# Kernel tuning notes

Hardware: AMD Instinct MI355X
Metric: run time of the kernel (lower is better)

The kernel has to match this reference:

```python
import jax, jax.numpy as jnp
import numpy as np

B, S, D = 8, 160, 256


def setup_inputs() -> dict:
    key = jax.random.key(0)
    kx, kw, kb = jax.random.split(key, 3)
    x = jax.random.normal(kx, (B, S, D), dtype=jnp.float32)
    # torch nn.Linear(2D, D): weight [D, 2D], bias [D]; store transposed W [2D, D]
    lim = 1.0 / np.sqrt(2 * D)
    W = jax.random.uniform(kw, (2 * D, D), minval=-lim, maxval=lim, dtype=jnp.float32)
    b = jax.random.uniform(kb, (D,), minval=-lim, maxval=lim, dtype=jnp.float32)
    return {"x": x, "W": W, "b": b}


def reference(x, W, b):
    Bsz, Ssz, Dsz = x.shape
    # all i<j pairs in the same order as the nested python loop (i outer, j inner)
    idx_i, idx_j = jnp.triu_indices(Ssz, k=1)  # each [P], P = S(S-1)/2
    # fc_rel(cat(x_i, x_j)) = x_i @ W[:D] + x_j @ W[D:] + b
    Wi, Wj = W[:Dsz], W[Dsz:]
    xa = jnp.einsum('bsd,de->bse', x, Wi)  # [B,S,D]
    xb = jnp.einsum('bsd,de->bse', x, Wj)  # [B,S,D]
    return xa[:, idx_i, :] + xb[:, idx_j, :] + b  # [B,P,D]
```

## Files before the change

### kernel.cpp

```cpp
#include <hip/hip_runtime.h>

#define SS 160
#define DD 256
#define BB 8
#define NPAIR 12720
#define M_TOT (BB * SS)
#define TOTROWS (BB * NPAIR)
#define NWAVES 8192

typedef float vfloat4 __attribute__((ext_vector_type(4)));

__global__ __launch_bounds__(512) void gemm_kernel(const float* __restrict__ x,
                                                   const float* __restrict__ W,
                                                   const float* __restrict__ bias,
                                                   float* __restrict__ y) {
    const int BM = 32, BN = 64, BK = 64;
    __shared__ float As[BK][BM + 1];
    __shared__ float Bs[BK][BN];

    const int n0 = blockIdx.x * BN;
    const int m0 = blockIdx.y * BM;
    const int half = (n0 >= DD) ? 1 : 0;
    const float* Wbase = W + (half ? DD * DD : 0);
    const int ncol0 = n0 - (half ? DD : 0);

    const int tid = threadIdx.x;
    const int tx = tid & 15;
    const int ty = tid >> 4;

    const int ar = tid >> 4;
    const int ac = (tid & 15) << 2;
    const int bkr = tid >> 4;
    const int bnc = (tid & 15) << 2;

    float acc[4] = {0.f, 0.f, 0.f, 0.f};

    for (int k0 = 0; k0 < DD; k0 += BK) {
        float4 av = *(const float4*)(x + (m0 + ar) * DD + k0 + ac);
        float4 b0 = *(const float4*)(Wbase + (k0 + bkr) * DD + ncol0 + bnc);
        float4 b1 = *(const float4*)(Wbase + (k0 + bkr + 32) * DD + ncol0 + bnc);
        __syncthreads();
        As[ac + 0][ar] = av.x;
        As[ac + 1][ar] = av.y;
        As[ac + 2][ar] = av.z;
        As[ac + 3][ar] = av.w;
        *(float4*)(&Bs[bkr][bnc])      = b0;
        *(float4*)(&Bs[bkr + 32][bnc]) = b1;
        __syncthreads();
#pragma unroll
        for (int kk = 0; kk < BK; ++kk) {
            float a = As[kk][ty];
            float4 bv = *(const float4*)(&Bs[kk][tx << 2]);
            acc[0] += a * bv.x; acc[1] += a * bv.y;
            acc[2] += a * bv.z; acc[3] += a * bv.w;
        }
    }

    float4 bias4 = make_float4(0.f, 0.f, 0.f, 0.f);
    if (!half) bias4 = *(const float4*)(bias + ncol0 + (tx << 2));

    float* yout = y + (half ? M_TOT * DD : 0);
    float4 r;
    r.x = acc[0] + bias4.x; r.y = acc[1] + bias4.y;
    r.z = acc[2] + bias4.z; r.w = acc[3] + bias4.w;
    *(float4*)(yout + (m0 + ty) * DD + ncol0 + (tx << 2)) = r;
}

__global__ __launch_bounds__(256) void expand_kernel(const float* __restrict__ y,
                                                     float* __restrict__ out) {
    const int gw   = (blockIdx.x << 2) + (threadIdx.x >> 6);
    const int lane = threadIdx.x & 63;

    int r0 = (int)(((long long)gw * TOTROWS) / NWAVES);
    int r1 = (int)(((long long)(gw + 1) * TOTROWS) / NWAVES);

    int b = (unsigned)r0 / NPAIR;
    int p = r0 - b * NPAIR;

    float disc = sqrtf((float)(101761 - 8 * p));
    int i = (int)((319.0f - disc) * 0.5f);
    if (i < 0) i = 0;
    if (i > SS - 2) i = SS - 2;
    while (i > 0 && (i * (2 * SS - 1 - i)) / 2 > p) --i;
    while (((i + 1) * (2 * SS - 2 - i)) / 2 <= p) ++i;
    int j = i + 1 + p - (i * (2 * SS - 1 - i)) / 2;

    const vfloat4* __restrict__ ya4 = (const vfloat4*)y;
    const vfloat4* __restrict__ yb4 = (const vfloat4*)(y + M_TOT * DD);
    vfloat4* po = (vfloat4*)out + ((long long)r0 << 6) + lane;

    int r = r0;
    while (r < r1) {
        vfloat4 va = ya4[((b * SS + i) << 6) + lane];
        const vfloat4* pb = yb4 + ((b * SS + j) << 6) + lane;
        int run = SS - j;
        if (run > r1 - r) run = r1 - r;
#pragma unroll 2
        for (int t = 0; t < run; ++t) {
            vfloat4 vb = pb[t * 64];
            vfloat4 o = va + vb;
            __builtin_nontemporal_store(o, po);
            po += 64;
        }
        r += run;
        ++i;
        if (i == SS - 1) { ++b; i = 0; }
        j = i + 1;
    }
}

extern "C" void kernel_launch(void* const* d_in, const int* in_sizes, int n_in,
                              void* d_out, int out_size, void* d_ws, size_t ws_size,
                              hipStream_t stream) {
    const float* x    = (const float*)d_in[0];
    const float* W    = (const float*)d_in[1];
    const float* bias = (const float*)d_in[2];
    float* y   = (float*)d_ws;
    float* out = (float*)d_out;

    dim3 gemm_grid(512 / 64, 1280 / 32);
    gemm_kernel<<<gemm_grid, 512, 0, stream>>>(x, W, bias, y);

    expand_kernel<<<NWAVES / 4, 256, 0, stream>>>(y, out);
}
```

Baseline: 133.9 us.

## Use 4x4 register tiling and double-buffered shared memory in projection GEMM

```diff
diff --git a/kernel.cpp b/kernel.cpp
--- a/kernel.cpp
+++ b/kernel.cpp
@@ -10,60 +10,99 @@
 
 typedef float vfloat4 __attribute__((ext_vector_type(4)));
 
-__global__ __launch_bounds__(512) void gemm_kernel(const float* __restrict__ x,
+__global__ __launch_bounds__(256) void gemm_kernel(const float* __restrict__ x,
                                                    const float* __restrict__ W,
                                                    const float* __restrict__ bias,
                                                    float* __restrict__ y) {
-    const int BM = 32, BN = 64, BK = 64;
-    __shared__ float As[BK][BM + 1];
-    __shared__ float Bs[BK][BN];
+    __shared__ float As[2][32][68];
+    __shared__ float Bs[2][32][64];
 
-    const int n0 = blockIdx.x * BN;
-    const int m0 = blockIdx.y * BM;
+    const int n0 = blockIdx.x * 64;
+    const int m0 = blockIdx.y * 64;
     const int half = (n0 >= DD) ? 1 : 0;
     const float* Wbase = W + (half ? DD * DD : 0);
     const int ncol0 = n0 - (half ? DD : 0);
 
     const int tid = threadIdx.x;
-    const int tx = tid & 15;
-    const int ty = tid >> 4;
+    const int tn = tid & 15;
+    const int tm = tid >> 4;
 
-    const int ar = tid >> 4;
-    const int ac = (tid & 15) << 2;
+    const int ar  = tid & 63;
+    const int af  = tid >> 6;
     const int bkr = tid >> 4;
     const int bnc = (tid & 15) << 2;
 
-    float acc[4] = {0.f, 0.f, 0.f, 0.f};
+    float acc[4][4] = {{0.f}};
 
-    for (int k0 = 0; k0 < DD; k0 += BK) {
-        float4 av = *(const float4*)(x + (m0 + ar) * DD + k0 + ac);
-        float4 b0 = *(const float4*)(Wbase + (k0 + bkr) * DD + ncol0 + bnc);
-        float4 b1 = *(const float4*)(Wbase + (k0 + bkr + 32) * DD + ncol0 + bnc);
-        __syncthreads();
-        As[ac + 0][ar] = av.x;
-        As[ac + 1][ar] = av.y;
-        As[ac + 2][ar] = av.z;
-        As[ac + 3][ar] = av.w;
-        *(float4*)(&Bs[bkr][bnc])      = b0;
-        *(float4*)(&Bs[bkr + 32][bnc]) = b1;
-        __syncthreads();
+    const float* xrow = x + (m0 + ar) * DD;
+
+    float4 pa0 = *(const float4*)(xrow + (af << 2));
+    float4 pa1 = *(const float4*)(xrow + (af << 2) + 16);
+    float4 pb0 = *(const float4*)(Wbase + bkr * DD + ncol0 + bnc);
+    float4 pb1 = *(const float4*)(Wbase + (bkr + 16) * DD + ncol0 + bnc);
+
+    As[0][(af << 2) + 0][ar]  = pa0.x;
+    As[0][(af << 2) + 1][ar]  = pa0.y;
+    As[0][(af << 2) + 2][ar]  = pa0.z;
+    As[0][(af << 2) + 3][ar]  = pa0.w;
+    As[0][(af << 2) + 16][ar] = pa1.x;
+    As[0][(af << 2) + 17][ar] = pa1.y;
+    As[0][(af << 2) + 18][ar] = pa1.z;
+    As[0][(af << 2) + 19][ar] = pa1.w;
+    *(float4*)(&Bs[0][bkr][bnc])      = pb0;
+    *(float4*)(&Bs[0][bkr + 16][bnc]) = pb1;
+    __syncthreads();
+
+    int cur = 0;
+    for (int t = 0; t < 8; ++t) {
+        if (t < 7) {
+            const int k0n = (t + 1) << 5;
+            pa0 = *(const float4*)(xrow + k0n + (af << 2));
+            pa1 = *(const float4*)(xrow + k0n + (af << 2) + 16);
+            pb0 = *(const float4*)(Wbase + (k0n + bkr) * DD + ncol0 + bnc);
+            pb1 = *(const float4*)(Wbase + (k0n + bkr + 16) * DD + ncol0 + bnc);
+        }
 #pragma unroll
-        for (int kk = 0; kk < BK; ++kk) {
-            float a = As[kk][ty];
-            float4 bv = *(const float4*)(&Bs[kk][tx << 2]);
-            acc[0] += a * bv.x; acc[1] += a * bv.y;
-            acc[2] += a * bv.z; acc[3] += a * bv.w;
+        for (int kk = 0; kk < 32; ++kk) {
+            float4 a4 = *(const float4*)(&As[cur][kk][tm << 2]);
+            float4 b4 = *(const float4*)(&Bs[cur][kk][tn << 2]);
+            acc[0][0] += a4.x * b4.x; acc[0][1] += a4.x * b4.y;
+            acc[0][2] += a4.x * b4.z; acc[0][3] += a4.x * b4.w;
+            acc[1][0] += a4.y * b4.x; acc[1][1] += a4.y * b4.y;
+            acc[1][2] += a4.y * b4.z; acc[1][3] += a4.y * b4.w;
+            acc[2][0] += a4.z * b4.x; acc[2][1] += a4.z * b4.y;
+            acc[2][2] += a4.z * b4.z; acc[2][3] += a4.z * b4.w;
+            acc[3][0] += a4.w * b4.x; acc[3][1] += a4.w * b4.y;
+            acc[3][2] += a4.w * b4.z; acc[3][3] += a4.w * b4.w;
+        }
+        if (t < 7) {
+            const int nb = cur ^ 1;
+            As[nb][(af << 2) + 0][ar]  = pa0.x;
+            As[nb][(af << 2) + 1][ar]  = pa0.y;
+            As[nb][(af << 2) + 2][ar]  = pa0.z;
+            As[nb][(af << 2) + 3][ar]  = pa0.w;
+            As[nb][(af << 2) + 16][ar] = pa1.x;
+            As[nb][(af << 2) + 17][ar] = pa1.y;
+            As[nb][(af << 2) + 18][ar] = pa1.z;
+            As[nb][(af << 2) + 19][ar] = pa1.w;
+            *(float4*)(&Bs[nb][bkr][bnc])      = pb0;
+            *(float4*)(&Bs[nb][bkr + 16][bnc]) = pb1;
+            __syncthreads();
+            cur = nb;
         }
     }
 
     float4 bias4 = make_float4(0.f, 0.f, 0.f, 0.f);
-    if (!half) bias4 = *(const float4*)(bias + ncol0 + (tx << 2));
+    if (!half) bias4 = *(const float4*)(bias + ncol0 + (tn << 2));
 
     float* yout = y + (half ? M_TOT * DD : 0);
-    float4 r;
-    r.x = acc[0] + bias4.x; r.y = acc[1] + bias4.y;
-    r.z = acc[2] + bias4.z; r.w = acc[3] + bias4.w;
-    *(float4*)(yout + (m0 + ty) * DD + ncol0 + (tx << 2)) = r;
+#pragma unroll
+    for (int i = 0; i < 4; ++i) {
+        float4 r;
+        r.x = acc[i][0] + bias4.x; r.y = acc[i][1] + bias4.y;
+        r.z = acc[i][2] + bias4.z; r.w = acc[i][3] + bias4.w;
+        *(float4*)(yout + (m0 + (tm << 2) + i) * DD + ncol0 + (tn << 2)) = r;
+    }
 }
 
 __global__ __launch_bounds__(256) void expand_kernel(const float* __restrict__ y,
@@ -118,8 +157,8 @@
     float* y   = (float*)d_ws;
     float* out = (float*)d_out;
 
-    dim3 gemm_grid(512 / 64, 1280 / 32);
-    gemm_kernel<<<gemm_grid, 512, 0, stream>>>(x, W, bias, y);
+    dim3 gemm_grid(512 / 64, 1280 / 64);
+    gemm_kernel<<<gemm_grid, 256, 0, stream>>>(x, W, bias, y);
 
     expand_kernel<<<NWAVES / 4, 256, 0, stream>>>(y, out);
 }
```

After: 131.3 us. Within noise of the previous version (-2.0%).
